# Performance work log

Hardware: AMD Instinct MI355X
Metric: run time of the kernel (lower is better)

Reference implementation:

```python
import jax, jax.numpy as jnp
import numpy as np

B, T, P = 4096, 128, 2
D_m = D_g = D_p = D_e = 256


def gru_cell(x, h, w_ih, w_hh, b_ih, b_hh):
    # PyTorch GRUCell math
    gi = x @ w_ih.T + b_ih          # [N, 3H]
    gh = h @ w_hh.T + b_hh          # [N, 3H]
    ir, iz, inn = jnp.split(gi, 3, axis=1)
    hr, hz, hn = jnp.split(gh, 3, axis=1)
    r = jax.nn.sigmoid(ir + hr)
    z = jax.nn.sigmoid(iz + hz)
    n = jnp.tanh(inn + r * hn)
    return (1.0 - z) * n + z * h


def _gru_params(key, in_dim, hid):
    k1, k2, k3, k4 = jax.random.split(key, 4)
    s = 1.0 / np.sqrt(hid)
    u = lambda k, shp: jax.random.uniform(k, shp, jnp.float32, -s, s)
    return u(k1, (3 * hid, in_dim)), u(k2, (3 * hid, hid)), u(k3, (3 * hid,)), u(k4, (3 * hid,))


def setup_inputs() -> dict:
    key = jax.random.key(0)
    ks = jax.random.split(key, 10)
    U = jax.random.normal(ks[0], (B, D_m), jnp.float32)
    qm_idx = jax.random.randint(ks[1], (B,), 0, P)
    g_hist = jax.random.normal(ks[2], (T, B, D_g), jnp.float32)
    q0 = jax.random.normal(ks[3], (B, P, D_p), jnp.float32)
    e0 = jax.random.normal(ks[4], (B, D_e), jnp.float32)
    wg = _gru_params(ks[5], D_m + D_p, D_g)
    wp = _gru_params(ks[6], D_m + D_g, D_p)
    we = _gru_params(ks[7], D_p, D_e)
    sa = 1.0 / np.sqrt(D_g)
    attn_w = jax.random.uniform(ks[8], (1, D_g), jnp.float32, -sa, sa)
    return {
        "U": U, "qm_idx": qm_idx, "g_hist": g_hist, "q0": q0, "e0": e0,
        "wg_ih": wg[0], "wg_hh": wg[1], "bg_ih": wg[2], "bg_hh": wg[3],
        "wp_ih": wp[0], "wp_hh": wp[1], "bp_ih": wp[2], "bp_hh": wp[3],
        "we_ih": we[0], "we_hh": we[1], "be_ih": we[2], "be_hh": we[3],
        "attn_w": attn_w,
    }


def reference(U, qm_idx, g_hist, q0, e0,
              wg_ih, wg_hh, bg_ih, bg_hh,
              wp_ih, wp_hh, bp_ih, bp_hh,
              we_ih, we_hh, be_ih, be_hh,
              attn_w):
    b_idx = jnp.arange(U.shape[0])
    qmask = jax.nn.one_hot(qm_idx, P, dtype=U.dtype)             # [B, P]
    # _select_parties: gather the speaking party's state
    q0_sel = q0[b_idx, qm_idx]                                    # [B, D_p]
    # global GRU step (g_hist non-empty -> hidden = g_hist[-1])
    g_ = gru_cell(jnp.concatenate([U, q0_sel], axis=1), g_hist[-1],
                  wg_ih, wg_hh, bg_ih, bg_hh)                     # [B, D_g]
    # SimpleAttention over history: softmax over time of a scalar score
    scale = jnp.einsum('tbd,od->tb', g_hist, attn_w)              # [T, B]
    alpha_t = jax.nn.softmax(scale, axis=0)                       # [T, B]
    c_ = jnp.einsum('tb,tbd->bd', alpha_t, g_hist)                # [B, D_g]
    alpha = alpha_t.T[:, None, :]                                 # [B, 1, T]
    # party GRU applied to every party slot
    U_c = jnp.concatenate([U, c_], axis=1)                        # [B, D_m+D_g]
    U_c_exp = jnp.broadcast_to(U_c[:, None, :], (U.shape[0], P, U_c.shape[1]))
    qs_ = gru_cell(U_c_exp.reshape(-1, D_m + D_g), q0.reshape(-1, D_p),
                   wp_ih, wp_hh, bp_ih, bp_hh).reshape(U.shape[0], P, D_p)
    # listener_state=False: listeners keep q0; speaker slot takes qs_
    qm = qmask[..., None]
    q_ = q0 * (1.0 - qm) + qs_ * qm                               # [B, P, D_p]
    # emotion GRU on the speaking party's updated state
    e_ = gru_cell(q_[b_idx, qm_idx], e0, we_ih, we_hh, be_ih, be_hh)  # [B, D_e]
    return g_, q_, e_, alpha
```

## Files before the change

### kernel.cpp

```cpp
#include <hip/hip_runtime.h>
#include <hip/hip_bf16.h>
#include <cstdint>
#include <cstddef>

#define B_N   4096
#define T_N   128
#define P_N   2
#define D     256
#define NG    768
#define BD    (B_N * D)

typedef __attribute__((ext_vector_type(4))) float f32x4;
typedef __attribute__((ext_vector_type(8))) short bf16x8;
typedef __attribute__((ext_vector_type(8))) unsigned short ushort8;

__device__ __forceinline__ unsigned short f2bf(float f) {
    __hip_bfloat16 h = __float2bfloat16(f);
    return *reinterpret_cast<unsigned short*>(&h);
}

struct CvtJobs {
    const float*     src[9];
    unsigned short*  dst[9];
    int              n[9];
};

__global__ __launch_bounds__(256) void cvt_batch(CvtJobs jobs)
{
    const int j = blockIdx.y;
    const int i = (blockIdx.x * 256 + threadIdx.x) * 8;
    if (i >= jobs.n[j]) return;
    const float4* s = reinterpret_cast<const float4*>(jobs.src[j] + i);
    const float4 v0 = s[0], v1 = s[1];
    ushort8 o = { f2bf(v0.x), f2bf(v0.y), f2bf(v0.z), f2bf(v0.w),
                  f2bf(v1.x), f2bf(v1.y), f2bf(v1.z), f2bf(v1.w) };
    *reinterpret_cast<ushort8*>(jobs.dst[j] + i) = o;
}

__global__ __launch_bounds__(256) void attn_kernel(
    const float* __restrict__ g_hist, const float* __restrict__ attn_w,
    unsigned short* __restrict__ c_bf, float* __restrict__ alpha_out)
{
    const int lane = threadIdx.x & 63;
    const int wid  = threadIdx.x >> 6;
    const int b    = blockIdx.x * 4 + wid;

    const float4 w4 = *reinterpret_cast<const float4*>(attn_w + lane * 4);
    const float* gbase = g_hist + (size_t)b * D + lane * 4;

    float  m = -INFINITY, l = 0.f;
    float4 acc = {0.f, 0.f, 0.f, 0.f};
    float  s0 = 0.f, s1 = 0.f;

    auto step = [&](int t, const float4& g) {
        float dot = g.x * w4.x + g.y * w4.y + g.z * w4.z + g.w * w4.w;
        #pragma unroll
        for (int off = 32; off >= 1; off >>= 1)
            dot += __shfl_xor(dot, off, 64);
        const float mn   = fmaxf(m, dot);
        const float corr = __expf(m - mn);
        const float p    = __expf(dot - mn);
        l = l * corr + p;
        acc.x = fmaf(p, g.x, acc.x * corr);
        acc.y = fmaf(p, g.y, acc.y * corr);
        acc.z = fmaf(p, g.z, acc.z * corr);
        acc.w = fmaf(p, g.w, acc.w * corr);
        m = mn;
        if ((t & 63) == lane) { if (t & 64) s1 = dot; else s0 = dot; }
    };

    for (int t = 0; t < T_N; t += 2) {
        const float4 g0 = *reinterpret_cast<const float4*>(gbase + (size_t)t * BD);
        const float4 g1 = *reinterpret_cast<const float4*>(gbase + (size_t)(t + 1) * BD);
        step(t, g0);
        step(t + 1, g1);
    }

    const float rl = 1.f / l;
    ushort4 cv = { f2bf(acc.x * rl), f2bf(acc.y * rl),
                   f2bf(acc.z * rl), f2bf(acc.w * rl) };
    *reinterpret_cast<ushort4*>(c_bf + (size_t)b * D + lane * 4) = cv;
    alpha_out[(size_t)b * T_N + lane]      = __expf(s0 - m) * rl;
    alpha_out[(size_t)b * T_N + 64 + lane] = __expf(s1 - m) * rl;
}

template<int MODE, int NI, int LDWI>
__global__ __launch_bounds__(256) void fused_gru(
    const unsigned short* __restrict__ A0,
    const unsigned short* __restrict__ A1,
    const unsigned short* __restrict__ Wi,
    const float* __restrict__ bi,
    const unsigned short* __restrict__ Ah,
    const unsigned short* __restrict__ Wh,
    const float* __restrict__ bh,
    const float* __restrict__ hsrc,
    const int*  __restrict__ qm,
    float* __restrict__ out_f32,
    unsigned short* __restrict__ out_bf)
{
    constexpr int NT = NI + 8;

    const int r0 = blockIdx.x * 128;
    const int c0 = blockIdx.y * 32;

    __shared__ unsigned short smem[3 * 8192];

    const int tid  = threadIdx.x;
    const int lane = tid & 63;
    const int wid  = tid >> 6;

    const int st_row = lane >> 2;
    const int st_p   = lane & 3;

    f32x4 accI[2][6] = {};
    f32x4 accH[2][6] = {};

    auto stage = [&](int step, int buf) {
        const unsigned short* Apart;
        const unsigned short* W;
        int kcolA, kcolW, ldw;
        if (step < NI) {
            const int kt = step * 32;
            Apart = (kt < D) ? A0 : A1;
            kcolA = kt & (D - 1);
            kcolW = kt;
            W     = Wi;
            ldw   = LDWI;
        } else {
            const int kt = (step - NI) * 32;
            Apart = Ah;
            kcolA = kt;
            kcolW = kt;
            W     = Wh;
            ldw   = D;
        }
        unsigned short* As = smem + buf * 8192;
        unsigned short* Ws = As + 4096;
        #pragma unroll
        for (int c = 0; c < 2; ++c) {
            const int row  = wid * 32 + c * 16 + st_row;
            const int scol = (st_p ^ ((row >> 1) & 3)) * 8;
            __builtin_amdgcn_global_load_lds(
                (const __attribute__((address_space(1))) void*)
                    (Apart + (size_t)(r0 + row) * D + kcolA + scol),
                (__attribute__((address_space(3))) void*)
                    (As + wid * 1024 + c * 512), 16, 0, 0);
            int grp = row >> 5; if (grp == 3) grp = 2;
            const int wrow = grp * 256 + c0 + (row & 31);
            __builtin_amdgcn_global_load_lds(
                (const __attribute__((address_space(1))) void*)
                    (W + (size_t)wrow * ldw + kcolW + scol),
                (__attribute__((address_space(3))) void*)
                    (Ws + wid * 1024 + c * 512), 16, 0, 0);
        }
    };

    auto compute = [&](int buf, f32x4 (&acc)[2][6]) {
        const unsigned short* As = smem + buf * 8192;
        const unsigned short* Ws = As + 4096;
        const int s  = lane >> 4;
        const int fr = lane & 15;
        bf16x8 a[2], b[6];
        #pragma unroll
        for (int m = 0; m < 2; ++m) {
            const int row = wid * 32 + m * 16 + fr;
            const int ph  = s ^ ((row >> 1) & 3);
            a[m] = *reinterpret_cast<const bf16x8*>(&As[row * 32 + ph * 8]);
        }
        #pragma unroll
        for (int j = 0; j < 6; ++j) {
            const int row = j * 16 + fr;
            const int ph  = s ^ ((row >> 1) & 3);
            b[j] = *reinterpret_cast<const bf16x8*>(&Ws[row * 32 + ph * 8]);
        }
        #pragma unroll
        for (int m = 0; m < 2; ++m)
            #pragma unroll
            for (int j = 0; j < 6; ++j)
                acc[m][j] = __builtin_amdgcn_mfma_f32_16x16x32_bf16(
                    a[m], b[j], acc[m][j], 0, 0, 0);
    };

    stage(0, 0);
    stage(1, 1);

    int cb = 0, ib = 2;
    for (int s = 0; s < NT; ++s) {
        if (s + 2 < NT) stage(s + 2, ib);
        const int rem = NT - 1 - s;
        if (rem >= 2)      asm volatile("s_waitcnt vmcnt(8)" ::: "memory");
        else if (rem == 1) asm volatile("s_waitcnt vmcnt(4)" ::: "memory");
        else               asm volatile("s_waitcnt vmcnt(0)" ::: "memory");
        __builtin_amdgcn_sched_barrier(0);
        __builtin_amdgcn_s_barrier();
        if (s < NI) compute(cb, accI);
        else        compute(cb, accH);
        __builtin_amdgcn_s_barrier();
        cb = (cb == 2) ? 0 : cb + 1;
        ib = (ib == 2) ? 0 : ib + 1;
    }

    const int cr = (lane >> 4) * 4;
    const int cc = lane & 15;
    #pragma unroll
    for (int m = 0; m < 2; ++m) {
        #pragma unroll
        for (int jj = 0; jj < 2; ++jj) {
            const int col = c0 + jj * 16 + cc;
            const float bir = bi[col],       bhr = bh[col];
            const float biz = bi[col + 256], bhz = bh[col + 256];
            const float bin = bi[col + 512], bhn = bh[col + 512];
            #pragma unroll
            for (int q = 0; q < 4; ++q) {
                const int row = r0 + wid * 32 + m * 16 + cr + q;
                const float ir  = accI[m][jj][q]     + bir;
                const float hr  = accH[m][jj][q]     + bhr;
                const float iz  = accI[m][jj + 2][q] + biz;
                const float hz  = accH[m][jj + 2][q] + bhz;
                const float in_ = accI[m][jj + 4][q] + bin;
                const float hn  = accH[m][jj + 4][q] + bhn;
                const float rg = 1.f / (1.f + __expf(-(ir + hr)));
                const float zg = 1.f / (1.f + __expf(-(iz + hz)));
                const float ng = tanhf(in_ + rg * hn);
                if (MODE == 1) {
                    const int p = qm[row];
                    const float hv  = hsrc[(size_t)row * 512 + (size_t)p * 256 + col];
                    const float ov  = hsrc[(size_t)row * 512 + (size_t)(1 - p) * 256 + col];
                    const float val = (1.f - zg) * ng + zg * hv;
                    out_f32[(size_t)row * 512 + (size_t)p * 256 + col]       = val;
                    out_f32[(size_t)row * 512 + (size_t)(1 - p) * 256 + col] = ov;
                    out_bf[(size_t)row * 256 + col] = f2bf(val);
                } else {
                    const float hv  = hsrc[(size_t)row * 256 + col];
                    const float val = (1.f - zg) * ng + zg * hv;
                    out_f32[(size_t)row * 256 + col] = val;
                }
            }
        }
    }
}

__global__ __launch_bounds__(256) void gather_q0(
    const float* __restrict__ q0, const int* __restrict__ qm,
    unsigned short* __restrict__ q0_sel_bf)
{
    const int i   = blockIdx.x * 256 + threadIdx.x;
    const int row = i >> 6;
    const int j   = (i & 63) * 4;
    const float4 v = *reinterpret_cast<const float4*>(
        q0 + ((size_t)row * P_N + qm[row]) * D + j);
    ushort4 bv = { f2bf(v.x), f2bf(v.y), f2bf(v.z), f2bf(v.w) };
    *reinterpret_cast<ushort4*>(q0_sel_bf + (size_t)row * D + j) = bv;
}

extern "C" void kernel_launch(void* const* d_in, const int* in_sizes, int n_in,
                              void* d_out, int out_size, void* d_ws, size_t ws_size,
                              hipStream_t stream)
{
    const float* U      = (const float*)d_in[0];
    const int*   qm     = (const int*)  d_in[1];
    const float* g_hist = (const float*)d_in[2];
    const float* q0     = (const float*)d_in[3];
    const float* e0     = (const float*)d_in[4];
    const float* wg_ih  = (const float*)d_in[5];
    const float* wg_hh  = (const float*)d_in[6];
    const float* bg_ih  = (const float*)d_in[7];
    const float* bg_hh  = (const float*)d_in[8];
    const float* wp_ih  = (const float*)d_in[9];
    const float* wp_hh  = (const float*)d_in[10];
    const float* bp_ih  = (const float*)d_in[11];
    const float* bp_hh  = (const float*)d_in[12];
    const float* we_ih  = (const float*)d_in[13];
    const float* we_hh  = (const float*)d_in[14];
    const float* be_ih  = (const float*)d_in[15];
    const float* be_hh  = (const float*)d_in[16];
    const float* attn_w = (const float*)d_in[17];

    float* out   = (float*)d_out;
    float* g_out = out;
    float* q_out = out + 1048576;
    float* e_out = out + 3145728;
    float* a_out = out + 4194304;

    unsigned short* bf = (unsigned short*)d_ws;
    unsigned short* U_bf     = bf;
    unsigned short* e0_bf    = bf + 1048576;
    unsigned short* glast_bf = bf + 2097152;
    unsigned short* q0sel_bf = bf + 3145728;
    unsigned short* c_bf     = bf + 4194304;
    unsigned short* qssel_bf = bf + 5242880;
    unsigned short* wgih_bf  = bf + 6291456;
    unsigned short* wpih_bf  = bf + 6684672;
    unsigned short* wghh_bf  = bf + 7077888;
    unsigned short* wphh_bf  = bf + 7274496;
    unsigned short* weih_bf  = bf + 7471104;
    unsigned short* wehh_bf  = bf + 7667712;

    const float* g_last = g_hist + (size_t)(T_N - 1) * BD;

    const dim3 blk(256);
    const dim3 gridGru(B_N / 128, D / 32);

    CvtJobs jobs;
    jobs.src[0] = wg_ih;  jobs.dst[0] = wgih_bf;  jobs.n[0] = NG * 512;
    jobs.src[1] = wg_hh;  jobs.dst[1] = wghh_bf;  jobs.n[1] = NG * 256;
    jobs.src[2] = wp_ih;  jobs.dst[2] = wpih_bf;  jobs.n[2] = NG * 512;
    jobs.src[3] = wp_hh;  jobs.dst[3] = wphh_bf;  jobs.n[3] = NG * 256;
    jobs.src[4] = we_ih;  jobs.dst[4] = weih_bf;  jobs.n[4] = NG * 256;
    jobs.src[5] = we_hh;  jobs.dst[5] = wehh_bf;  jobs.n[5] = NG * 256;
    jobs.src[6] = U;      jobs.dst[6] = U_bf;     jobs.n[6] = B_N * D;
    jobs.src[7] = e0;     jobs.dst[7] = e0_bf;    jobs.n[7] = B_N * D;
    jobs.src[8] = g_last; jobs.dst[8] = glast_bf; jobs.n[8] = B_N * D;
    cvt_batch<<<dim3(B_N * D / 8 / 256, 9), blk, 0, stream>>>(jobs);

    gather_q0<<<B_N * D / 4 / 256, blk, 0, stream>>>(q0, qm, q0sel_bf);
    attn_kernel<<<B_N / 4, blk, 0, stream>>>(g_hist, attn_w, c_bf, a_out);

    fused_gru<0, 16, 512><<<gridGru, blk, 0, stream>>>(
        U_bf, q0sel_bf, wgih_bf, bg_ih,
        glast_bf, wghh_bf, bg_hh,
        g_last, nullptr, g_out, nullptr);

    fused_gru<1, 16, 512><<<gridGru, blk, 0, stream>>>(
        U_bf, c_bf, wpih_bf, bp_ih,
        q0sel_bf, wphh_bf, bp_hh,
        q0, qm, q_out, qssel_bf);

    fused_gru<0, 8, 256><<<gridGru, blk, 0, stream>>>(
        qssel_bf, nullptr, weih_bf, be_ih,
        e0_bf, wehh_bf, be_hh,
        e0, nullptr, e_out, nullptr);
}
```

Before: 166.7 us.

## Merge conversion, gather and attention kernels; run global and party GRUs together

The six launches become three. One grid-stride kernel now does the weight and activation bf16 conversions, the q0 gather and the attention pass. The independent global and party GRU GEMMs share a single 512-block launch, and the emotion GRU keeps its own kernel. The aim is to cut launch overhead and the gaps between dependent kernels, and to fill the device better with two GEMMs side by side. In exchange, the attention work in each block now waits behind its share of the conversion loops.

Measured after the change: 162.0 us. -2.8%, faster.

```diff
diff --git a/kernel.cpp b/kernel.cpp
--- a/kernel.cpp
+++ b/kernel.cpp
@@ -9,6 +9,8 @@
 #define D     256
 #define NG    768
 #define BD    (B_N * D)
+#define AGRID 1024
+#define AGSIZE (AGRID * 256)
 
 typedef __attribute__((ext_vector_type(4))) float f32x4;
 typedef __attribute__((ext_vector_type(8))) short bf16x8;
@@ -19,34 +21,70 @@
     return *reinterpret_cast<unsigned short*>(&h);
 }
 
-struct CvtJobs {
-    const float*     src[9];
-    unsigned short*  dst[9];
-    int              n[9];
+struct AttnParams {
+    const float *U, *g_hist, *q0, *e0;
+    const int   *qm;
+    const float *wg_ih, *wg_hh, *wp_ih, *wp_hh, *we_ih, *we_hh;
+    const float *attn_w;
+    float *a_out;
+    unsigned short *U_bf, *e0_bf, *glast_bf, *q0sel_bf, *c_bf;
+    unsigned short *wgih_bf, *wpih_bf, *wghh_bf, *wphh_bf, *weih_bf, *wehh_bf;
 };
 
-__global__ __launch_bounds__(256) void cvt_batch(CvtJobs jobs)
-{
-    const int j = blockIdx.y;
-    const int i = (blockIdx.x * 256 + threadIdx.x) * 8;
-    if (i >= jobs.n[j]) return;
-    const float4* s = reinterpret_cast<const float4*>(jobs.src[j] + i);
-    const float4 v0 = s[0], v1 = s[1];
-    ushort8 o = { f2bf(v0.x), f2bf(v0.y), f2bf(v0.z), f2bf(v0.w),
-                  f2bf(v1.x), f2bf(v1.y), f2bf(v1.z), f2bf(v1.w) };
-    *reinterpret_cast<ushort8*>(jobs.dst[j] + i) = o;
-}
-
-__global__ __launch_bounds__(256) void attn_kernel(
-    const float* __restrict__ g_hist, const float* __restrict__ attn_w,
-    unsigned short* __restrict__ c_bf, float* __restrict__ alpha_out)
-{
-    const int lane = threadIdx.x & 63;
-    const int wid  = threadIdx.x >> 6;
-    const int b    = blockIdx.x * 4 + wid;
-
-    const float4 w4 = *reinterpret_cast<const float4*>(attn_w + lane * 4);
-    const float* gbase = g_hist + (size_t)b * D + lane * 4;
+struct GPParams {
+    const unsigned short *U_bf, *q0sel_bf, *glast_bf, *c_bf;
+    const unsigned short *wgih_bf, *wghh_bf, *wpih_bf, *wphh_bf;
+    const float *bg_ih, *bg_hh, *bp_ih, *bp_hh;
+    const float *g_last, *q0;
+    const int *qm;
+    float *g_out, *q_out;
+    unsigned short *qssel_bf;
+};
+
+__device__ __forceinline__ void cvt8(
+    const float* __restrict__ src, unsigned short* __restrict__ dst,
+    int n8, int gtid)
+{
+    for (int i = gtid; i < n8; i += AGSIZE) {
+        const float4* s = reinterpret_cast<const float4*>(src + i * 8);
+        const float4 v0 = s[0], v1 = s[1];
+        ushort8 o = { f2bf(v0.x), f2bf(v0.y), f2bf(v0.z), f2bf(v0.w),
+                      f2bf(v1.x), f2bf(v1.y), f2bf(v1.z), f2bf(v1.w) };
+        *reinterpret_cast<ushort8*>(dst + i * 8) = o;
+    }
+}
+
+__global__ __launch_bounds__(256) void attn_fused(AttnParams p)
+{
+    const int tid  = threadIdx.x;
+    const int lane = tid & 63;
+    const int wid  = tid >> 6;
+    const int gtid = blockIdx.x * 256 + tid;
+
+    const float* g_last = p.g_hist + (size_t)(T_N - 1) * BD;
+
+    cvt8(p.wg_ih, p.wgih_bf, NG * 512 / 8, gtid);
+    cvt8(p.wg_hh, p.wghh_bf, NG * 256 / 8, gtid);
+    cvt8(p.wp_ih, p.wpih_bf, NG * 512 / 8, gtid);
+    cvt8(p.wp_hh, p.wphh_bf, NG * 256 / 8, gtid);
+    cvt8(p.we_ih, p.weih_bf, NG * 256 / 8, gtid);
+    cvt8(p.we_hh, p.wehh_bf, NG * 256 / 8, gtid);
+    cvt8(p.U,     p.U_bf,     B_N * D / 8, gtid);
+    cvt8(p.e0,    p.e0_bf,    B_N * D / 8, gtid);
+    cvt8(g_last,  p.glast_bf, B_N * D / 8, gtid);
+    for (int i = gtid; i < B_N * D / 4; i += AGSIZE) {
+        const int row = i >> 6;
+        const int j   = (i & 63) * 4;
+        const float4 v = *reinterpret_cast<const float4*>(
+            p.q0 + ((size_t)row * P_N + p.qm[row]) * D + j);
+        ushort4 bv = { f2bf(v.x), f2bf(v.y), f2bf(v.z), f2bf(v.w) };
+        *reinterpret_cast<ushort4*>(p.q0sel_bf + (size_t)row * D + j) = bv;
+    }
+
+    const int b = blockIdx.x * 4 + wid;
+
+    const float4 w4 = *reinterpret_cast<const float4*>(p.attn_w + lane * 4);
+    const float* gbase = p.g_hist + (size_t)b * D + lane * 4;
 
     float  m = -INFINITY, l = 0.f;
     float4 acc = {0.f, 0.f, 0.f, 0.f};
@@ -59,12 +97,12 @@
             dot += __shfl_xor(dot, off, 64);
         const float mn   = fmaxf(m, dot);
         const float corr = __expf(m - mn);
-        const float p    = __expf(dot - mn);
-        l = l * corr + p;
-        acc.x = fmaf(p, g.x, acc.x * corr);
-        acc.y = fmaf(p, g.y, acc.y * corr);
-        acc.z = fmaf(p, g.z, acc.z * corr);
-        acc.w = fmaf(p, g.w, acc.w * corr);
+        const float pr   = __expf(dot - mn);
+        l = l * corr + pr;
+        acc.x = fmaf(pr, g.x, acc.x * corr);
+        acc.y = fmaf(pr, g.y, acc.y * corr);
+        acc.z = fmaf(pr, g.z, acc.z * corr);
+        acc.w = fmaf(pr, g.w, acc.w * corr);
         m = mn;
         if ((t & 63) == lane) { if (t & 64) s1 = dot; else s0 = dot; }
     };
@@ -79,36 +117,26 @@
     const float rl = 1.f / l;
     ushort4 cv = { f2bf(acc.x * rl), f2bf(acc.y * rl),
                    f2bf(acc.z * rl), f2bf(acc.w * rl) };
-    *reinterpret_cast<ushort4*>(c_bf + (size_t)b * D + lane * 4) = cv;
-    alpha_out[(size_t)b * T_N + lane]      = __expf(s0 - m) * rl;
-    alpha_out[(size_t)b * T_N + 64 + lane] = __expf(s1 - m) * rl;
+    *reinterpret_cast<ushort4*>(p.c_bf + (size_t)b * D + lane * 4) = cv;
+    p.a_out[(size_t)b * T_N + lane]      = __expf(s0 - m) * rl;
+    p.a_out[(size_t)b * T_N + 64 + lane] = __expf(s1 - m) * rl;
 }
 
 template<int MODE, int NI, int LDWI>
-__global__ __launch_bounds__(256) void fused_gru(
+__device__ __forceinline__ void gru_body(
+    int r0, int c0, unsigned short* smem, int tid,
     const unsigned short* __restrict__ A0,
     const unsigned short* __restrict__ A1,
-    const unsigned short* __restrict__ Wi,
-    const float* __restrict__ bi,
+    const unsigned short* __restrict__ Wi, const float* __restrict__ bi,
     const unsigned short* __restrict__ Ah,
-    const unsigned short* __restrict__ Wh,
-    const float* __restrict__ bh,
-    const float* __restrict__ hsrc,
-    const int*  __restrict__ qm,
-    float* __restrict__ out_f32,
-    unsigned short* __restrict__ out_bf)
+    const unsigned short* __restrict__ Wh, const float* __restrict__ bh,
+    const float* __restrict__ hsrc, const int* __restrict__ qm,
+    float* __restrict__ out_f32, unsigned short* __restrict__ out_bf)
 {
     constexpr int NT = NI + 8;
 
-    const int r0 = blockIdx.x * 128;
-    const int c0 = blockIdx.y * 32;
-
-    __shared__ unsigned short smem[3 * 8192];
-
-    const int tid  = threadIdx.x;
     const int lane = tid & 63;
     const int wid  = tid >> 6;
-
     const int st_row = lane >> 2;
     const int st_p   = lane & 3;
 
@@ -128,11 +156,7 @@
             ldw   = LDWI;
         } else {
             const int kt = (step - NI) * 32;
-            Apart = Ah;
-            kcolA = kt;
-            kcolW = kt;
-            W     = Wh;
-            ldw   = D;
+            Apart = Ah; kcolA = kt; kcolW = kt; W = Wh; ldw = D;
         }
         unsigned short* As = smem + buf * 8192;
         unsigned short* Ws = As + 4096;
@@ -240,17 +264,43 @@
     }
 }
 
-__global__ __launch_bounds__(256) void gather_q0(
-    const float* __restrict__ q0, const int* __restrict__ qm,
-    unsigned short* __restrict__ q0_sel_bf)
-{
-    const int i   = blockIdx.x * 256 + threadIdx.x;
-    const int row = i >> 6;
-    const int j   = (i & 63) * 4;
-    const float4 v = *reinterpret_cast<const float4*>(
-        q0 + ((size_t)row * P_N + qm[row]) * D + j);
-    ushort4 bv = { f2bf(v.x), f2bf(v.y), f2bf(v.z), f2bf(v.w) };
-    *reinterpret_cast<ushort4*>(q0_sel_bf + (size_t)row * D + j) = bv;
+__global__ __launch_bounds__(256) void gp_gru(GPParams p)
+{
+    __shared__ unsigned short smem[3 * 8192];
+    const int tid = threadIdx.x;
+    const int bid = blockIdx.x;
+
+    if (bid < 256) {
+        const int r0 = (bid & 31) * 128, c0 = (bid >> 5) * 32;
+        gru_body<0, 16, 512>(r0, c0, smem, tid,
+            p.U_bf, p.q0sel_bf, p.wgih_bf, p.bg_ih,
+            p.glast_bf, p.wghh_bf, p.bg_hh,
+            p.g_last, nullptr, p.g_out, nullptr);
+    } else {
+        const int gb = bid - 256;
+        const int r0 = (gb & 31) * 128, c0 = (gb >> 5) * 32;
+        gru_body<1, 16, 512>(r0, c0, smem, tid,
+            p.U_bf, p.c_bf, p.wpih_bf, p.bp_ih,
+            p.q0sel_bf, p.wphh_bf, p.bp_hh,
+            p.q0, p.qm, p.q_out, p.qssel_bf);
+    }
+}
+
+__global__ __launch_bounds__(256) void e_gru(
+    const unsigned short* __restrict__ qssel_bf,
+    const unsigned short* __restrict__ weih_bf, const float* __restrict__ be_ih,
+    const unsigned short* __restrict__ e0_bf,
+    const unsigned short* __restrict__ wehh_bf, const float* __restrict__ be_hh,
+    const float* __restrict__ e0, float* __restrict__ e_out)
+{
+    __shared__ unsigned short smem[3 * 8192];
+    const int tid = threadIdx.x;
+    const int bid = blockIdx.x;
+    const int r0 = (bid & 31) * 128, c0 = (bid >> 5) * 32;
+    gru_body<0, 8, 256>(r0, c0, smem, tid,
+        qssel_bf, nullptr, weih_bf, be_ih,
+        e0_bf, wehh_bf, be_hh,
+        e0, nullptr, e_out, nullptr);
 }
 
 extern "C" void kernel_launch(void* const* d_in, const int* in_sizes, int n_in,
@@ -298,36 +348,28 @@
 
     const float* g_last = g_hist + (size_t)(T_N - 1) * BD;
 
+    AttnParams ap;
+    ap.U = U; ap.g_hist = g_hist; ap.q0 = q0; ap.e0 = e0; ap.qm = qm;
+    ap.wg_ih = wg_ih; ap.wg_hh = wg_hh; ap.wp_ih = wp_ih; ap.wp_hh = wp_hh;
+    ap.we_ih = we_ih; ap.we_hh = we_hh; ap.attn_w = attn_w;
+    ap.a_out = a_out;
+    ap.U_bf = U_bf; ap.e0_bf = e0_bf; ap.glast_bf = glast_bf;
+    ap.q0sel_bf = q0sel_bf; ap.c_bf = c_bf;
+    ap.wgih_bf = wgih_bf; ap.wpih_bf = wpih_bf; ap.wghh_bf = wghh_bf;
+    ap.wphh_bf = wphh_bf; ap.weih_bf = weih_bf; ap.wehh_bf = wehh_bf;
+
+    GPParams gp;
+    gp.U_bf = U_bf; gp.q0sel_bf = q0sel_bf; gp.glast_bf = glast_bf;
+    gp.c_bf = c_bf;
+    gp.wgih_bf = wgih_bf; gp.wghh_bf = wghh_bf;
+    gp.wpih_bf = wpih_bf; gp.wphh_bf = wphh_bf;
+    gp.bg_ih = bg_ih; gp.bg_hh = bg_hh; gp.bp_ih = bp_ih; gp.bp_hh = bp_hh;
+    gp.g_last = g_last; gp.q0 = q0; gp.qm = qm;
+    gp.g_out = g_out; gp.q_out = q_out; gp.qssel_bf = qssel_bf;
+
     const dim3 blk(256);
-    const dim3 gridGru(B_N / 128, D / 32);
-
-    CvtJobs jobs;
-    jobs.src[0] = wg_ih;  jobs.dst[0] = wgih_bf;  jobs.n[0] = NG * 512;
-    jobs.src[1] = wg_hh;  jobs.dst[1] = wghh_bf;  jobs.n[1] = NG * 256;
-    jobs.src[2] = wp_ih;  jobs.dst[2] = wpih_bf;  jobs.n[2] = NG * 512;
-    jobs.src[3] = wp_hh;  jobs.dst[3] = wphh_bf;  jobs.n[3] = NG * 256;
-    jobs.src[4] = we_ih;  jobs.dst[4] = weih_bf;  jobs.n[4] = NG * 256;
-    jobs.src[5] = we_hh;  jobs.dst[5] = wehh_bf;  jobs.n[5] = NG * 256;
-    jobs.src[6] = U;      jobs.dst[6] = U_bf;     jobs.n[6] = B_N * D;
-    jobs.src[7] = e0;     jobs.dst[7] = e0_bf;    jobs.n[7] = B_N * D;
-    jobs.src[8] = g_last; jobs.dst[8] = glast_bf; jobs.n[8] = B_N * D;
-    cvt_batch<<<dim3(B_N * D / 8 / 256, 9), blk, 0, stream>>>(jobs);
-
-    gather_q0<<<B_N * D / 4 / 256, blk, 0, stream>>>(q0, qm, q0sel_bf);
-    attn_kernel<<<B_N / 4, blk, 0, stream>>>(g_hist, attn_w, c_bf, a_out);
-
-    fused_gru<0, 16, 512><<<gridGru, blk, 0, stream>>>(
-        U_bf, q0sel_bf, wgih_bf, bg_ih,
-        glast_bf, wghh_bf, bg_hh,
-        g_last, nullptr, g_out, nullptr);
-
-    fused_gru<1, 16, 512><<<gridGru, blk, 0, stream>>>(
-        U_bf, c_bf, wpih_bf, bp_ih,
-        q0sel_bf, wphh_bf, bp_hh,
-        q0, qm, q_out, qssel_bf);
-
-    fused_gru<0, 8, 256><<<gridGru, blk, 0, stream>>>(
-        qssel_bf, nullptr, weih_bf, be_ih,
-        e0_bf, wehh_bf, be_hh,
-        e0, nullptr, e_out, nullptr);
-}
+    attn_fused<<<AGRID, blk, 0, stream>>>(ap);
+    gp_gru<<<512, blk, 0, stream>>>(gp);
+    e_gru<<<256, blk, 0, stream>>>(
+        qssel_bf, weih_bf, be_ih, e0_bf, wehh_bf, be_hh, e0, e_out);
+}
```
